# Kernel optimization log

Measured on AMD Instinct MI355X. Metric: run time of the kernel, lower is better.

The kernel has to match this reference:

```python
import jax, jax.numpy as jnp
import numpy as np

B, S, NX, NH = 4, 2048, 1024, 16
HD = NX // NH
MASKED_BIAS = -10000.0


def setup_inputs() -> dict:
    key = jax.random.key(0)
    k1, k2, k3 = jax.random.split(key, 3)
    x = jax.random.normal(k1, (B, S, NX), dtype=jnp.float32)
    w_attn = jax.random.normal(k2, (NX, 3 * NX), dtype=jnp.float32) * 0.02
    b_attn = jnp.zeros((3 * NX,), dtype=jnp.float32)
    w_proj = jax.random.normal(k3, (NX, NX), dtype=jnp.float32) * 0.02
    b_proj = jnp.zeros((NX,), dtype=jnp.float32)
    return {"x": x, "w_attn": w_attn, "b_attn": b_attn, "w_proj": w_proj, "b_proj": b_proj}


def reference(x, w_attn, b_attn, w_proj, b_proj):
    b, s, nx = x.shape
    # c_attn (HF Conv1D): y = x @ W + b
    qkv = x @ w_attn + b_attn                      # [b, s, 3*nx]
    q, k, v = jnp.split(qkv, 3, axis=-1)
    # split heads -> [b, h, s, d]
    q = q.reshape(b, s, NH, HD).transpose(0, 2, 1, 3)
    k = k.reshape(b, s, NH, HD).transpose(0, 2, 1, 3)
    v = v.reshape(b, s, NH, HD).transpose(0, 2, 1, 3)
    # scaled scores, scale by 1/sqrt(head_dim) since scale=True
    w = jnp.einsum('bhqd,bhkd->bhqk', q, k) / jnp.sqrt(jnp.asarray(HD, x.dtype))
    # tril causal mask (bias buffer slice for nd == ns == s)
    causal = jnp.tril(jnp.ones((s, s), dtype=bool))
    w = jnp.where(causal, w, jnp.asarray(MASKED_BIAS, w.dtype))
    w = jax.nn.softmax(w, axis=-1)
    a = jnp.einsum('bhqk,bhkd->bhqd', w, v)        # [b, h, s, d]
    # merge heads -> [b, s, nx]
    a = a.transpose(0, 2, 1, 3).reshape(b, s, nx)
    # c_proj
    a = a @ w_proj + b_proj
    return a
```

## Files before the change

### kernel.cpp

```cpp
#include <hip/hip_runtime.h>
#include <stdint.h>

#define BATCH 4
#define SEQ 2048
#define NX 1024
#define NHEAD 16
#define HDIM 64
#define NTOK (BATCH * SEQ)
#define QKV_LD (3 * NX)

typedef __bf16 bf16_t;
typedef __bf16 bf16x8 __attribute__((ext_vector_type(8)));
typedef __bf16 bf16x4 __attribute__((ext_vector_type(4)));
typedef float  f32x4  __attribute__((ext_vector_type(4)));

#define GLOAD_LDS16(g, l) __builtin_amdgcn_global_load_lds( \
    (const __attribute__((address_space(1))) void*)(g),     \
    (__attribute__((address_space(3))) void*)(l), 16, 0, 0)

#define MFMA16(a, b, c) __builtin_amdgcn_mfma_f32_16x16x32_bf16((a), (b), (c), 0, 0, 0)

#define WAIT_VM4_BAR() do { \
    asm volatile("s_waitcnt vmcnt(4)" ::: "memory"); \
    __builtin_amdgcn_s_barrier(); } while (0)
#define WAIT_VM0_BAR() do { \
    asm volatile("s_waitcnt vmcnt(0)" ::: "memory"); \
    __builtin_amdgcn_s_barrier(); } while (0)

__global__ __launch_bounds__(256) void k_cast_bf16(const float* __restrict__ in,
                                                   bf16_t* __restrict__ out, int n4) {
  int stride = gridDim.x * blockDim.x;
  for (int i = blockIdx.x * blockDim.x + threadIdx.x; i < n4; i += stride) {
    f32x4 v = ((const f32x4*)in)[i];
    bf16x4 o;
    o[0] = (bf16_t)v[0]; o[1] = (bf16_t)v[1];
    o[2] = (bf16_t)v[2]; o[3] = (bf16_t)v[3];
    ((bf16x4*)out)[i] = o;
  }
}

__global__ __launch_bounds__(256) void k_transpose_cast(const float* __restrict__ in,
                                                        bf16_t* __restrict__ out,
                                                        int K, int N) {
  __shared__ float tile[32][33];
  const int kb = blockIdx.x * 32, nb = blockIdx.y * 32;
  const int tx = threadIdx.x & 31;
  const int ty = (threadIdx.x >> 5) * 4;
#pragma unroll
  for (int i = 0; i < 4; i++)
    tile[ty + i][tx] = in[(size_t)(kb + ty + i) * N + nb + tx];
  __syncthreads();
#pragma unroll
  for (int i = 0; i < 4; i++)
    out[(size_t)(nb + ty + i) * K + kb + tx] = (bf16_t)tile[tx][ty + i];
}

__global__ __launch_bounds__(256) void k_vtrans(const bf16_t* __restrict__ qkv,
                                                bf16_t* __restrict__ vt) {
  __shared__ bf16_t tile[32][33];
  const int s0 = blockIdx.x * 32;
  const int d0 = blockIdx.y * 32;
  const int bh = blockIdx.z;
  const int b = bh >> 4, h = bh & 15;
  const bf16_t* src = qkv + (size_t)b * SEQ * QKV_LD + 2 * NX + h * HDIM;
  const int tx = threadIdx.x & 31;
  const int ty = (threadIdx.x >> 5) * 4;
#pragma unroll
  for (int i = 0; i < 4; i++)
    tile[ty + i][tx] = src[(size_t)(s0 + ty + i) * QKV_LD + d0 + tx];
  __syncthreads();
  bf16_t* dst = vt + (size_t)bh * HDIM * SEQ;
#pragma unroll
  for (int i = 0; i < 4; i++)
    dst[(size_t)(d0 + ty + i) * SEQ + s0 + tx] = tile[tx][ty + i];
}

template <int OUT_BF16>
__global__ __launch_bounds__(256) void k_gemm_bt(const bf16_t* __restrict__ A,
                                                 const bf16_t* __restrict__ Bt,
                                                 const float* __restrict__ bias,
                                                 void* __restrict__ Cout,
                                                 int M, int N, int K) {
  __shared__ __align__(16) bf16_t lsA[2][128 * 32];
  __shared__ __align__(16) bf16_t lsB[2][128 * 32];
  const int tid  = threadIdx.x;
  const int lane = tid & 63;
  const int wid  = tid >> 6;
  const int wr   = wid >> 1, wc = wid & 1;
  const int m0 = blockIdx.x * 128, n0 = blockIdx.y * 128;

  const int srow = tid >> 2;
  const int scol = ((tid & 3) ^ (srow & 3)) * 8;
  const bf16_t* Ap = A  + (size_t)(m0 + srow) * K + scol;
  const bf16_t* Bp = Bt + (size_t)(n0 + srow) * K + scol;
  const int wbase = (tid & ~63) * 8;

  f32x4 acc[4][4];
#pragma unroll
  for (int i = 0; i < 4; i++)
#pragma unroll
    for (int j = 0; j < 4; j++) acc[i][j] = (f32x4){0.f, 0.f, 0.f, 0.f};

  const int fr = lane & 15;
  const int g2 = lane >> 4;
  const int rslot = (g2 ^ (fr & 3)) * 8;

  auto stage = [&](int buf, int k0) {
    GLOAD_LDS16(Ap + k0,                  &lsA[buf][wbase]);
    GLOAD_LDS16(Ap + (size_t)64 * K + k0, &lsA[buf][2048 + wbase]);
    GLOAD_LDS16(Bp + k0,                  &lsB[buf][wbase]);
    GLOAD_LDS16(Bp + (size_t)64 * K + k0, &lsB[buf][2048 + wbase]);
  };

  const int nk = K >> 5;
  stage(0, 0);
  WAIT_VM0_BAR();

  for (int kt = 0; kt < nk; kt++) {
    const int cur = kt & 1;
    if (kt + 1 < nk) stage(cur ^ 1, (kt + 1) * 32);
    bf16x8 af[4], bfr[4];
#pragma unroll
    for (int mf = 0; mf < 4; mf++)
      af[mf] = *(const bf16x8*)&lsA[cur][(wr * 64 + mf * 16 + fr) * 32 + rslot];
#pragma unroll
    for (int nf = 0; nf < 4; nf++)
      bfr[nf] = *(const bf16x8*)&lsB[cur][(wc * 64 + nf * 16 + fr) * 32 + rslot];
#pragma unroll
    for (int mf = 0; mf < 4; mf++)
#pragma unroll
      for (int nf = 0; nf < 4; nf++)
        acc[mf][nf] = MFMA16(af[mf], bfr[nf], acc[mf][nf]);
    if (kt + 1 < nk) WAIT_VM0_BAR();
  }

  const int col = lane & 15, rb = (lane >> 4) * 4;
#pragma unroll
  for (int mf = 0; mf < 4; mf++) {
#pragma unroll
    for (int nf = 0; nf < 4; nf++) {
      const int gm = m0 + wr * 64 + mf * 16 + rb;
      const int gn = n0 + wc * 64 + nf * 16 + col;
      const float bv = bias[gn];
#pragma unroll
      for (int r = 0; r < 4; r++) {
        float v = acc[mf][nf][r] + bv;
        if (OUT_BF16)
          ((bf16_t*)Cout)[(size_t)(gm + r) * N + gn] = (bf16_t)v;
        else
          ((float*)Cout)[(size_t)(gm + r) * N + gn] = v;
      }
    }
  }
}

__global__ __launch_bounds__(256, 2) void k_attn(const bf16_t* __restrict__ qkv,
                                                 const bf16_t* __restrict__ vt,
                                                 bf16_t* __restrict__ attout) {
  __shared__ __align__(16) bf16_t lsK[3][64 * 64];
  __shared__ __align__(16) bf16_t lsV[3][64 * 64];
  const int tid = threadIdx.x, lane = tid & 63, w = tid >> 6;
  const int blk = blockIdx.x;
  const int bh  = (blk & 7) * 8 + ((blk >> 3) & 7);
  const int qsb = (0x32104567u >> ((blk >> 6) << 2)) & 7;
  const int b = bh >> 4, h = bh & 15;
  const bf16_t* Qb  = qkv + (size_t)b * SEQ * QKV_LD + h * HDIM;
  const bf16_t* Kb  = Qb + NX;
  const bf16_t* Vtb = vt + (size_t)bh * HDIM * SEQ;

  const int fr = lane & 15, g2 = lane >> 4;
  const int kb8 = g2 * 8;
  const int permA = (fr & 3) + 8 * (fr >> 2);

  auto stage = [&](int buf, int kv0) {
#pragma unroll
    for (int s = 0; s < 2; s++) {
      const int i = w * 128 + s * 64 + lane;
      const int row = i >> 3, slot = i & 7;
      const int sk = (row & 3) | (((row >> 3) & 1) << 2);
      GLOAD_LDS16(Kb + (size_t)(kv0 + row) * QKV_LD + ((slot ^ sk) << 3),
                  &lsK[buf][(w * 128 + s * 64) * 8]);
      GLOAD_LDS16(Vtb + (size_t)row * SEQ + kv0 + ((slot ^ (row & 7)) << 3),
                  &lsV[buf][(w * 128 + s * 64) * 8]);
    }
  };

  const int wb = qsb * 256 + w * 64;
  const int kv_last = wb;
  const int nst = qsb * 4 + 4;

  bf16x8 bq[4][2];
#pragma unroll
  for (int g = 0; g < 4; g++)
#pragma unroll
    for (int kf = 0; kf < 2; kf++) {
      bf16x8 t = *(const bf16x8*)&Qb[(size_t)(wb + g * 16 + fr) * QKV_LD + kf * 32 + kb8];
#pragma unroll
      for (int jj = 0; jj < 8; jj++) t[jj] = (bf16_t)((float)t[jj] * 0.1803368801f);
      bq[g][kf] = t;
    }

  float l_run[4] = {0.f, 0.f, 0.f, 0.f};
  f32x4 o[4][4];
#pragma unroll
  for (int g = 0; g < 4; g++)
#pragma unroll
    for (int d = 0; d < 4; d++) o[g][d] = (f32x4){0.f, 0.f, 0.f, 0.f};

  stage(0, 0);
  stage(1, 64);
  asm volatile("s_waitcnt vmcnt(4)" ::: "memory");
  __builtin_amdgcn_s_barrier();

  for (int st = 0; st < nst; st++) {
    const int kv0 = st * 64;
    const int cur = st % 3;
    if (st + 2 < nst) stage((st + 2) % 3, (st + 2) * 64);
    if (kv0 <= kv_last) {
      bf16x8 ak[2][2][2];
#pragma unroll
      for (int sub = 0; sub < 2; sub++)
#pragma unroll
        for (int ab = 0; ab < 2; ab++)
#pragma unroll
          for (int kf = 0; kf < 2; kf++) {
            const int row = sub * 32 + ab * 4 + permA;
            const int sk = (row & 3) | (((row >> 3) & 1) << 2);
            const int c = kf * 4 + g2;
            ak[sub][ab][kf] = *(const bf16x8*)&lsK[cur][row * 64 + ((c ^ sk) << 3)];
          }
      bf16x8 vbf[4][2];
#pragma unroll
      for (int df = 0; df < 4; df++)
#pragma unroll
        for (int hh = 0; hh < 2; hh++) {
          const int row = df * 16 + fr;
          const int c = hh * 4 + g2;
          vbf[df][hh] = *(const bf16x8*)&lsV[cur][row * 64 + ((c ^ (row & 7)) << 3)];
        }
      const int masked = (kv0 == kv_last);
#pragma unroll
      for (int g = 0; g < 4; g++) {
        f32x4 sAB[2][2];
        __builtin_amdgcn_s_setprio(1);
#pragma unroll
        for (int sub = 0; sub < 2; sub++)
#pragma unroll
          for (int ab = 0; ab < 2; ab++) {
            f32x4 s0 = (f32x4){0.f, 0.f, 0.f, 0.f};
            s0 = MFMA16(ak[sub][ab][0], bq[g][0], s0);
            s0 = MFMA16(ak[sub][ab][1], bq[g][1], s0);
            sAB[sub][ab] = s0;
          }
        __builtin_amdgcn_s_setprio(0);
        float sv[16];
#pragma unroll
        for (int sub = 0; sub < 2; sub++)
#pragma unroll
          for (int r = 0; r < 4; r++) {
            sv[sub * 8 + r]     = sAB[sub][0][r];
            sv[sub * 8 + 4 + r] = sAB[sub][1][r];
          }
        if (masked) {
          const int q_abs = wb + g * 16 + fr;
#pragma unroll
          for (int sub = 0; sub < 2; sub++)
#pragma unroll
            for (int r = 0; r < 4; r++) {
              if (kv0 + sub * 32 + g2 * 8 + r     > q_abs) sv[sub * 8 + r]     = -1e30f;
              if (kv0 + sub * 32 + g2 * 8 + 4 + r > q_abs) sv[sub * 8 + 4 + r] = -1e30f;
            }
        }
        float tsum = 0.f;
        bf16_t pb[16];
#pragma unroll
        for (int jj = 0; jj < 16; jj++) {
          float pv = exp2f(sv[jj]);
          tsum += pv;
          pb[jj] = (bf16_t)pv;
        }
        l_run[g] += tsum;
        bf16x8 pa0, pa1;
#pragma unroll
        for (int jj = 0; jj < 8; jj++) { pa0[jj] = pb[jj]; pa1[jj] = pb[8 + jj]; }
        __builtin_amdgcn_s_setprio(1);
#pragma unroll
        for (int df = 0; df < 4; df++) {
          o[g][df] = MFMA16(pa0, vbf[df][0], o[g][df]);
          o[g][df] = MFMA16(pa1, vbf[df][1], o[g][df]);
        }
        __builtin_amdgcn_s_setprio(0);
      }
    }
    if (st + 1 < nst) {
      if (st + 2 < nst) WAIT_VM4_BAR(); else WAIT_VM0_BAR();
    }
  }

#pragma unroll
  for (int g = 0; g < 4; g++) {
    float lt = l_run[g];
    lt += __shfl_xor(lt, 16);
    lt += __shfl_xor(lt, 32);
    const float inv = 1.f / lt;
#pragma unroll
    for (int r = 0; r < 4; r++) {
      const float iv = __shfl(inv, g2 * 4 + r);
      const int tok = b * SEQ + wb + g * 16 + g2 * 4 + r;
#pragma unroll
      for (int df = 0; df < 4; df++)
        attout[(size_t)tok * NX + h * HDIM + df * 16 + fr] = (bf16_t)(o[g][df][r] * iv);
    }
  }
}

extern "C" void kernel_launch(void* const* d_in, const int* in_sizes, int n_in,
                              void* d_out, int out_size, void* d_ws, size_t ws_size,
                              hipStream_t stream) {
  const float* x      = (const float*)d_in[0];
  const float* w_attn = (const float*)d_in[1];
  const float* b_attn = (const float*)d_in[2];
  const float* w_proj = (const float*)d_in[3];
  const float* b_proj = (const float*)d_in[4];

  char* ws = (char*)d_ws;
  bf16_t* xb  = (bf16_t*)ws;
  bf16_t* qkv = (bf16_t*)(ws + (16u << 20));
  bf16_t* wab = (bf16_t*)(ws + (64u << 20));
  bf16_t* vt  = (bf16_t*)(ws + (64u << 20));
  bf16_t* wpb = (bf16_t*)(ws + (80u << 20));
  bf16_t* att = xb;

  k_cast_bf16<<<2048, 256, 0, stream>>>(x, xb, NTOK * NX / 4);
  k_transpose_cast<<<dim3(NX / 32, (3 * NX) / 32), 256, 0, stream>>>(w_attn, wab, NX, 3 * NX);
  k_gemm_bt<1><<<dim3(NTOK / 128, (3 * NX) / 128), 256, 0, stream>>>(
      xb, wab, b_attn, (void*)qkv, NTOK, 3 * NX, NX);
  k_vtrans<<<dim3(SEQ / 32, HDIM / 32, BATCH * NHEAD), 256, 0, stream>>>(qkv, vt);
  k_transpose_cast<<<dim3(NX / 32, NX / 32), 256, 0, stream>>>(w_proj, wpb, NX, NX);
  k_attn<<<BATCH * NHEAD * 8, 256, 0, stream>>>(qkv, vt, att);
  k_gemm_bt<0><<<dim3(NTOK / 128, NX / 128), 256, 0, stream>>>(
      att, wpb, b_proj, d_out, NTOK, NX, NX);
}
```

Measured before the change: 193.5 us.

## Fuse V transpose into QKV GEMM epilogue and drop separate transpose kernel

The QKV projection GEMM now writes V tiles through LDS directly into a transposed per-head layout inside the qkv buffer, and the attention kernel reads V from there. This removes the separate V-transpose kernel and its extra pass over global memory. The GEMMs also drop the LDS XOR swizzle and replace explicit waitcnt barriers with __syncthreads. The attention block-to-query-tile ordering is simplified. The unswizzled LDS layout risks bank conflicts, and the barrier change relies on __syncthreads covering the async LDS loads.

```diff
diff --git a/kernel.cpp b/kernel.cpp
--- a/kernel.cpp
+++ b/kernel.cpp
@@ -21,11 +21,12 @@
 #define MFMA16(a, b, c) __builtin_amdgcn_mfma_f32_16x16x32_bf16((a), (b), (c), 0, 0, 0)
 
 #define WAIT_VM4_BAR() do { \
-    asm volatile("s_waitcnt vmcnt(4)" ::: "memory"); \
+    asm volatile("s_waitcnt vmcnt(4) lgkmcnt(0)" ::: "memory"); \
     __builtin_amdgcn_s_barrier(); } while (0)
 #define WAIT_VM0_BAR() do { \
-    asm volatile("s_waitcnt vmcnt(0)" ::: "memory"); \
+    asm volatile("s_waitcnt vmcnt(0) lgkmcnt(0)" ::: "memory"); \
     __builtin_amdgcn_s_barrier(); } while (0)
+
 
 __global__ __launch_bounds__(256) void k_cast_bf16(const float* __restrict__ in,
                                                    bf16_t* __restrict__ out, int n4) {
@@ -55,31 +56,116 @@
     out[(size_t)(nb + ty + i) * K + kb + tx] = (bf16_t)tile[tx][ty + i];
 }
 
-__global__ __launch_bounds__(256) void k_vtrans(const bf16_t* __restrict__ qkv,
-                                                bf16_t* __restrict__ vt) {
-  __shared__ bf16_t tile[32][33];
-  const int s0 = blockIdx.x * 32;
-  const int d0 = blockIdx.y * 32;
-  const int bh = blockIdx.z;
-  const int b = bh >> 4, h = bh & 15;
-  const bf16_t* src = qkv + (size_t)b * SEQ * QKV_LD + 2 * NX + h * HDIM;
-  const int tx = threadIdx.x & 31;
-  const int ty = (threadIdx.x >> 5) * 4;
+__global__ __launch_bounds__(256) void k_gemm_qkv(const bf16_t* __restrict__ A,
+                                                  const bf16_t* __restrict__ Bt,
+                                                  const float* __restrict__ bias,
+                                                  bf16_t* __restrict__ qkv,
+                                                  int M, int N, int K) {
+  __shared__ __align__(16) bf16_t lsPool[2][2][128 * 32];
+  auto* lsA = lsPool[0];
+  auto* lsB = lsPool[1];
+  const int tid  = threadIdx.x;
+  const int lane = tid & 63;
+  const int wid  = tid >> 6;
+  const int wr   = wid >> 1, wc = wid & 1;
+  const int m0 = blockIdx.x * 128, n0 = blockIdx.y * 128;
+
+  const int srow = tid >> 2;
+  const int scol = (tid & 3) * 8;
+  const bf16_t* Ap = A  + (size_t)(m0 + srow) * K + scol;
+  const bf16_t* Bp = Bt + (size_t)(n0 + srow) * K + scol;
+  const int wbase = (tid & ~63) * 8;
+
+  f32x4 acc[4][4];
 #pragma unroll
   for (int i = 0; i < 4; i++)
-    tile[ty + i][tx] = src[(size_t)(s0 + ty + i) * QKV_LD + d0 + tx];
+#pragma unroll
+    for (int j = 0; j < 4; j++) acc[i][j] = (f32x4){0.f, 0.f, 0.f, 0.f};
+
+  const int fr = lane & 15;
+  const int kb = (lane >> 4) * 8;
+
+  auto stage = [&](int buf, int k0) {
+    GLOAD_LDS16(Ap + k0,                  &lsA[buf][wbase]);
+    GLOAD_LDS16(Ap + (size_t)64 * K + k0, &lsA[buf][2048 + wbase]);
+    GLOAD_LDS16(Bp + k0,                  &lsB[buf][wbase]);
+    GLOAD_LDS16(Bp + (size_t)64 * K + k0, &lsB[buf][2048 + wbase]);
+  };
+
+  stage(0, 0);
   __syncthreads();
-  bf16_t* dst = vt + (size_t)bh * HDIM * SEQ;
-#pragma unroll
-  for (int i = 0; i < 4; i++)
-    dst[(size_t)(d0 + ty + i) * SEQ + s0 + tx] = tile[tx][ty + i];
-}
-
-template <int OUT_BF16>
+  const int nk = K >> 5;
+  for (int kt = 0; kt < nk; kt++) {
+    const int cur = kt & 1;
+    if (kt + 1 < nk) stage(cur ^ 1, (kt + 1) * 32);
+    bf16x8 af[4], bfr[4];
+#pragma unroll
+    for (int mf = 0; mf < 4; mf++)
+      af[mf] = *(const bf16x8*)&lsA[cur][(wr * 64 + mf * 16 + fr) * 32 + kb];
+#pragma unroll
+    for (int nf = 0; nf < 4; nf++)
+      bfr[nf] = *(const bf16x8*)&lsB[cur][(wc * 64 + nf * 16 + fr) * 32 + kb];
+#pragma unroll
+    for (int mf = 0; mf < 4; mf++)
+#pragma unroll
+      for (int nf = 0; nf < 4; nf++)
+        acc[mf][nf] = MFMA16(af[mf], bfr[nf], acc[mf][nf]);
+    __syncthreads();
+  }
+
+  const int col = lane & 15, rb = (lane >> 4) * 4;
+
+  if (n0 < 2 * NX) {
+#pragma unroll
+    for (int mf = 0; mf < 4; mf++)
+#pragma unroll
+      for (int nf = 0; nf < 4; nf++) {
+        const int gm = m0 + wr * 64 + mf * 16 + rb;
+        const int gn = n0 + wc * 64 + nf * 16 + col;
+        const float bv = bias[gn];
+#pragma unroll
+        for (int r = 0; r < 4; r++)
+          qkv[(size_t)(gm + r) * QKV_LD + gn] = (bf16_t)(acc[mf][nf][r] + bv);
+      }
+  } else {
+    bf16_t* lt = &lsPool[0][0][0];
+    const int bb  = m0 >> 11;
+    const int m0s = m0 & 2047;
+    const int rr = tid >> 4, cc = tid & 15;
+#pragma unroll
+    for (int p = 0; p < 2; p++) {
+      __syncthreads();
+      if (wc == p) {
+#pragma unroll
+        for (int mf = 0; mf < 4; mf++)
+#pragma unroll
+          for (int nf = 0; nf < 4; nf++) {
+            const float bv = bias[n0 + wc * 64 + nf * 16 + col];
+            bf16x4 v4;
+#pragma unroll
+            for (int r = 0; r < 4; r++) v4[r] = (bf16_t)(acc[mf][nf][r] + bv);
+            *(bf16x4*)&lt[(nf * 16 + col) * 136 + wr * 64 + mf * 16 + rb] = v4;
+          }
+      }
+      __syncthreads();
+      const int hh = ((n0 - 2 * NX) >> 6) + p;
+#pragma unroll
+      for (int it = 0; it < 4; it++) {
+        const int nn = it * 16 + rr;
+        bf16x8 v = *(const bf16x8*)&lt[nn * 136 + cc * 8];
+        const size_t dst = (size_t)bb * SEQ * QKV_LD +
+                           (size_t)((hh * 64 + nn) * 2 + (m0s >> 10)) * QKV_LD +
+                           2 * NX + (m0s & 1023) + cc * 8;
+        *(bf16x8*)&qkv[dst] = v;
+      }
+    }
+  }
+}
+
 __global__ __launch_bounds__(256) void k_gemm_bt(const bf16_t* __restrict__ A,
                                                  const bf16_t* __restrict__ Bt,
                                                  const float* __restrict__ bias,
-                                                 void* __restrict__ Cout,
+                                                 float* __restrict__ Cout,
                                                  int M, int N, int K) {
   __shared__ __align__(16) bf16_t lsA[2][128 * 32];
   __shared__ __align__(16) bf16_t lsB[2][128 * 32];
@@ -90,7 +176,7 @@
   const int m0 = blockIdx.x * 128, n0 = blockIdx.y * 128;
 
   const int srow = tid >> 2;
-  const int scol = ((tid & 3) ^ (srow & 3)) * 8;
+  const int scol = (tid & 3) * 8;
   const bf16_t* Ap = A  + (size_t)(m0 + srow) * K + scol;
   const bf16_t* Bp = Bt + (size_t)(n0 + srow) * K + scol;
   const int wbase = (tid & ~63) * 8;
@@ -102,8 +188,7 @@
     for (int j = 0; j < 4; j++) acc[i][j] = (f32x4){0.f, 0.f, 0.f, 0.f};
 
   const int fr = lane & 15;
-  const int g2 = lane >> 4;
-  const int rslot = (g2 ^ (fr & 3)) * 8;
+  const int kb = (lane >> 4) * 8;
 
   auto stage = [&](int buf, int k0) {
     GLOAD_LDS16(Ap + k0,                  &lsA[buf][wbase]);
@@ -112,26 +197,25 @@
     GLOAD_LDS16(Bp + (size_t)64 * K + k0, &lsB[buf][2048 + wbase]);
   };
 
+  stage(0, 0);
+  __syncthreads();
   const int nk = K >> 5;
-  stage(0, 0);
-  WAIT_VM0_BAR();
-
   for (int kt = 0; kt < nk; kt++) {
     const int cur = kt & 1;
     if (kt + 1 < nk) stage(cur ^ 1, (kt + 1) * 32);
     bf16x8 af[4], bfr[4];
 #pragma unroll
     for (int mf = 0; mf < 4; mf++)
-      af[mf] = *(const bf16x8*)&lsA[cur][(wr * 64 + mf * 16 + fr) * 32 + rslot];
+      af[mf] = *(const bf16x8*)&lsA[cur][(wr * 64 + mf * 16 + fr) * 32 + kb];
 #pragma unroll
     for (int nf = 0; nf < 4; nf++)
-      bfr[nf] = *(const bf16x8*)&lsB[cur][(wc * 64 + nf * 16 + fr) * 32 + rslot];
+      bfr[nf] = *(const bf16x8*)&lsB[cur][(wc * 64 + nf * 16 + fr) * 32 + kb];
 #pragma unroll
     for (int mf = 0; mf < 4; mf++)
 #pragma unroll
       for (int nf = 0; nf < 4; nf++)
         acc[mf][nf] = MFMA16(af[mf], bfr[nf], acc[mf][nf]);
-    if (kt + 1 < nk) WAIT_VM0_BAR();
+    __syncthreads();
   }
 
   const int col = lane & 15, rb = (lane >> 4) * 4;
@@ -143,30 +227,25 @@
       const int gn = n0 + wc * 64 + nf * 16 + col;
       const float bv = bias[gn];
 #pragma unroll
-      for (int r = 0; r < 4; r++) {
-        float v = acc[mf][nf][r] + bv;
-        if (OUT_BF16)
-          ((bf16_t*)Cout)[(size_t)(gm + r) * N + gn] = (bf16_t)v;
-        else
-          ((float*)Cout)[(size_t)(gm + r) * N + gn] = v;
-      }
+      for (int r = 0; r < 4; r++)
+        Cout[(size_t)(gm + r) * N + gn] = acc[mf][nf][r] + bv;
     }
   }
 }
 
 __global__ __launch_bounds__(256, 2) void k_attn(const bf16_t* __restrict__ qkv,
-                                                 const bf16_t* __restrict__ vt,
                                                  bf16_t* __restrict__ attout) {
   __shared__ __align__(16) bf16_t lsK[3][64 * 64];
   __shared__ __align__(16) bf16_t lsV[3][64 * 64];
   const int tid = threadIdx.x, lane = tid & 63, w = tid >> 6;
   const int blk = blockIdx.x;
-  const int bh  = (blk & 7) * 8 + ((blk >> 3) & 7);
-  const int qsb = (0x32104567u >> ((blk >> 6) << 2)) & 7;
+  const int xcd = blk & 7, idx = blk >> 3;
+  const int bh  = xcd * 8 + (idx & 7);
+  const int qsb = 7 - (idx >> 3);
   const int b = bh >> 4, h = bh & 15;
-  const bf16_t* Qb  = qkv + (size_t)b * SEQ * QKV_LD + h * HDIM;
-  const bf16_t* Kb  = Qb + NX;
-  const bf16_t* Vtb = vt + (size_t)bh * HDIM * SEQ;
+  const bf16_t* Qb = qkv + (size_t)b * SEQ * QKV_LD + h * HDIM;
+  const bf16_t* Kb = Qb + NX;
+  const bf16_t* Vs = qkv + (size_t)b * SEQ * QKV_LD + 2 * NX;
 
   const int fr = lane & 15, g2 = lane >> 4;
   const int kb8 = g2 * 8;
@@ -180,7 +259,8 @@
       const int sk = (row & 3) | (((row >> 3) & 1) << 2);
       GLOAD_LDS16(Kb + (size_t)(kv0 + row) * QKV_LD + ((slot ^ sk) << 3),
                   &lsK[buf][(w * 128 + s * 64) * 8]);
-      GLOAD_LDS16(Vtb + (size_t)row * SEQ + kv0 + ((slot ^ (row & 7)) << 3),
+      GLOAD_LDS16(Vs + (size_t)((h * 64 + row) * 2 + (kv0 >> 10)) * QKV_LD +
+                      (kv0 & 1023) + ((slot ^ (row & 7)) << 3),
                   &lsV[buf][(w * 128 + s * 64) * 8]);
     }
   };
@@ -327,17 +407,15 @@
   bf16_t* xb  = (bf16_t*)ws;
   bf16_t* qkv = (bf16_t*)(ws + (16u << 20));
   bf16_t* wab = (bf16_t*)(ws + (64u << 20));
-  bf16_t* vt  = (bf16_t*)(ws + (64u << 20));
-  bf16_t* wpb = (bf16_t*)(ws + (80u << 20));
+  bf16_t* wpb = (bf16_t*)(ws + (70u << 20));
   bf16_t* att = xb;
 
   k_cast_bf16<<<2048, 256, 0, stream>>>(x, xb, NTOK * NX / 4);
   k_transpose_cast<<<dim3(NX / 32, (3 * NX) / 32), 256, 0, stream>>>(w_attn, wab, NX, 3 * NX);
-  k_gemm_bt<1><<<dim3(NTOK / 128, (3 * NX) / 128), 256, 0, stream>>>(
-      xb, wab, b_attn, (void*)qkv, NTOK, 3 * NX, NX);
-  k_vtrans<<<dim3(SEQ / 32, HDIM / 32, BATCH * NHEAD), 256, 0, stream>>>(qkv, vt);
+  k_gemm_qkv<<<dim3(NTOK / 128, (3 * NX) / 128), 256, 0, stream>>>(
+      xb, wab, b_attn, qkv, NTOK, 3 * NX, NX);
   k_transpose_cast<<<dim3(NX / 32, NX / 32), 256, 0, stream>>>(w_proj, wpb, NX, NX);
-  k_attn<<<BATCH * NHEAD * 8, 256, 0, stream>>>(qkv, vt, att);
-  k_gemm_bt<0><<<dim3(NTOK / 128, NX / 128), 256, 0, stream>>>(
-      att, wpb, b_proj, d_out, NTOK, NX, NX);
-}
+  k_attn<<<BATCH * NHEAD * 8, 256, 0, stream>>>(qkv, att);
+  k_gemm_bt<<<dim3(NTOK / 128, NX / 128), 256, 0, stream>>>(
+      att, wpb, b_proj, (float*)d_out, NTOK, NX, NX);
+}
```

Result: faster. 186.5 us, median of 2 (-3.6%).
